# Kernel tuning notes

Measured on AMD Instinct MI355X. Metric: run time of the kernel, lower is better.

## Reference

```python
import jax, jax.numpy as jnp
import numpy as np

DIM, HEADS, MLP_RATIO = 384, 6, 4.0
HEAD_DIM = DIM // HEADS
HID = int(DIM * MLP_RATIO)
EPS = 1e-5


def _layer_norm(x, g, b):
    m = jnp.mean(x, axis=-1, keepdims=True)
    v = jnp.mean(jnp.square(x - m), axis=-1, keepdims=True)
    return (x - m) * jax.lax.rsqrt(v + EPS) * g + b


def setup_inputs() -> dict:
    key = jax.random.key(0)
    ks = jax.random.split(key, 16)
    B, N, C = 4, 2048, DIM
    s = 0.02
    return {
        "x": jax.random.normal(ks[0], (B, N, C), dtype=jnp.float32),
        "ln1_g": jnp.ones((C,), jnp.float32),
        "ln1_b": jnp.zeros((C,), jnp.float32),
        "qkv_w": jax.random.normal(ks[1], (C, 3 * C), jnp.float32) * s,  # [in, out]
        "qkv_b": jnp.zeros((3 * C,), jnp.float32),
        "proj_w": jax.random.normal(ks[2], (C, C), jnp.float32) * s,
        "proj_b": jnp.zeros((C,), jnp.float32),
        "ln2_g": jnp.ones((C,), jnp.float32),
        "ln2_b": jnp.zeros((C,), jnp.float32),
        "fc1_w": jax.random.normal(ks[3], (C, HID), jnp.float32) * s,
        "fc1_b": jnp.zeros((HID,), jnp.float32),
        "fc2_w": jax.random.normal(ks[4], (HID, C), jnp.float32) * s,
        "fc2_b": jnp.zeros((C,), jnp.float32),
    }


def reference(x, ln1_g, ln1_b, qkv_w, qkv_b, proj_w, proj_b,
              ln2_g, ln2_b, fc1_w, fc1_b, fc2_w, fc2_b):
    B, N, C = x.shape
    scale = HEAD_DIM ** (-0.5)

    # --- attention branch (pre-norm) ---
    h = _layer_norm(x, ln1_g, ln1_b)
    qkv = (h @ qkv_w + qkv_b).reshape(B, N, 3, HEADS, HEAD_DIM)
    qkv = jnp.transpose(qkv, (2, 0, 3, 1, 4))  # [3, B, H, N, D]
    q, k, v = qkv[0], qkv[1], qkv[2]
    attn = jnp.einsum("bhnd,bhmd->bhnm", q, k) * scale
    attn = jax.nn.softmax(attn, axis=-1)
    out = jnp.einsum("bhnm,bhmd->bhnd", attn, v)
    out = jnp.transpose(out, (0, 2, 1, 3)).reshape(B, N, C)
    x = x + (out @ proj_w + proj_b)

    # --- MLP branch (pre-norm) ---
    h = _layer_norm(x, ln2_g, ln2_b)
    h = jax.nn.gelu(h @ fc1_w + fc1_b, approximate=False)
    x = x + (h @ fc2_w + fc2_b)
    return x
```

## Files before the change

### kernel.cpp

```cpp
#include <hip/hip_runtime.h>

typedef unsigned short u16;
typedef unsigned int u32;
typedef __bf16 bf16x8_t __attribute__((ext_vector_type(8)));
typedef float f32x4 __attribute__((ext_vector_type(4)));
typedef float f32x16 __attribute__((ext_vector_type(16)));

__device__ __forceinline__ u16 f2b(float f) {
  union { float f; u32 u; } v; v.f = f;
  u32 r = v.u + 0x7fffu + ((v.u >> 16) & 1u);
  return (u16)(r >> 16);
}

__device__ __forceinline__ u32 pkbf(float a, float b) {
  union { __bf16 h[2]; u32 u; } v;
  v.h[0] = (__bf16)a; v.h[1] = (__bf16)b;
  return v.u;
}

__device__ __forceinline__ f32x4 mfma16(uint4 a, uint4 b, f32x4 c) {
  return __builtin_amdgcn_mfma_f32_16x16x32_bf16(
      __builtin_bit_cast(bf16x8_t, a), __builtin_bit_cast(bf16x8_t, b), c, 0, 0, 0);
}

__device__ __forceinline__ f32x16 mfma32(uint4 a, uint4 b, f32x16 c) {
  return __builtin_amdgcn_mfma_f32_32x32x16_bf16(
      __builtin_bit_cast(bf16x8_t, a), __builtin_bit_cast(bf16x8_t, b), c, 0, 0, 0);
}

__device__ __forceinline__ void plswap(u32& a, u32& b) {
  asm("v_permlane32_swap_b32 %0, %1" : "+v"(a), "+v"(b));
}

__device__ __forceinline__ void load_lds16(const void* g, void* l) {
  __builtin_amdgcn_global_load_lds(
      (const __attribute__((address_space(1))) unsigned int*)g,
      (__attribute__((address_space(3))) unsigned int*)l, 16, 0, 0);
}

template <int N>
__device__ __forceinline__ void waitvm() {
  if constexpr (N == 0) asm volatile("s_waitcnt vmcnt(0)" ::: "memory");
  else if constexpr (N == 2) asm volatile("s_waitcnt vmcnt(2)" ::: "memory");
  else if constexpr (N == 4) asm volatile("s_waitcnt vmcnt(4)" ::: "memory");
  else if constexpr (N == 6) asm volatile("s_waitcnt vmcnt(6)" ::: "memory");
  else asm volatile("s_waitcnt vmcnt(8)" ::: "memory");
}

__global__ __launch_bounds__(256) void convT4_k(
    const float* __restrict__ w0, u16* __restrict__ t0_,
    const float* __restrict__ w1, u16* __restrict__ t1_,
    const float* __restrict__ w2, u16* __restrict__ t2_,
    const float* __restrict__ w3, u16* __restrict__ t3_) {
  __shared__ u16 L[64][68];
  int tile = blockIdx.x, tid = threadIdx.x;
  const float* w; u16* wt; int K, N, rel;
  if (tile < 108)      { w = w0; wt = t0_; K = 384;  N = 1152; rel = tile; }
  else if (tile < 144) { w = w1; wt = t1_; K = 384;  N = 384;  rel = tile - 108; }
  else if (tile < 288) { w = w2; wt = t2_; K = 384;  N = 1536; rel = tile - 144; }
  else                 { w = w3; wt = t3_; K = 1536; N = 384;  rel = tile - 288; }
  int ntx = N >> 6;
  int tk = (rel / ntx) << 6, tn = (rel - (rel / ntx) * ntx) << 6;

  int r = tid >> 2, c0 = (tid & 3) << 4;
  const float* src = w + (size_t)(tk + r) * N + tn + c0;
#pragma unroll
  for (int j = 0; j < 16; j += 4) {
    float4 a = *(const float4*)(src + j);
    L[r][c0 + j + 0] = f2b(a.x);
    L[r][c0 + j + 1] = f2b(a.y);
    L[r][c0 + j + 2] = f2b(a.z);
    L[r][c0 + j + 3] = f2b(a.w);
  }
  __syncthreads();
  int n = tid >> 2, k0 = (tid & 3) << 4;
  u16 tmp[16];
#pragma unroll
  for (int j = 0; j < 16; j++) tmp[j] = L[k0 + j][n];
  u16* dst = wt + (size_t)(tn + n) * K + tk + k0;
  *(uint4*)dst = *(const uint4*)(tmp);
  *(uint4*)(dst + 8) = *(const uint4*)(tmp + 8);
}

__global__ __launch_bounds__(256) void ln_k(const float* __restrict__ x,
                                            const float* __restrict__ g,
                                            const float* __restrict__ bta,
                                            u16* __restrict__ out) {
  int lane = threadIdx.x & 63, wid = threadIdx.x >> 6;
  int row = blockIdx.x * 4 + wid;
  const float* xr = x + (size_t)row * 384;
  float v[6];
  float s = 0.f;
#pragma unroll
  for (int i = 0; i < 6; i++) { v[i] = xr[i * 64 + lane]; s += v[i]; }
#pragma unroll
  for (int off = 32; off >= 1; off >>= 1) s += __shfl_xor(s, off);
  float mean = s * (1.0f / 384.0f);
  float vs = 0.f;
#pragma unroll
  for (int i = 0; i < 6; i++) { float d = v[i] - mean; vs += d * d; }
#pragma unroll
  for (int off = 32; off >= 1; off >>= 1) vs += __shfl_xor(vs, off);
  float rstd = rsqrtf(vs * (1.0f / 384.0f) + 1e-5f);
  u16* orow = out + (size_t)row * 384;
#pragma unroll
  for (int i = 0; i < 6; i++) {
    int c = i * 64 + lane;
    orow[c] = f2b((v[i] - mean) * rstd * g[c] + bta[c]);
  }
}

template <int EPI, int MR, int NR>
__global__ __launch_bounds__(256, 3) void gemm_k(
    const u16* __restrict__ A, const u16* __restrict__ Bt,
    const float* __restrict__ bias, const float* __restrict__ res,
    void* __restrict__ outp, int M, int Nn, int K,
    u16* __restrict__ qp, u16* __restrict__ kp, u16* __restrict__ vtp) {
  constexpr int BMt = MR * 32;
  constexpr int BNt = NR * 32;
  constexpr int AW = MR / 2;
  constexpr int BW = NR / 2;
  __shared__ __align__(16) u16 As[3][BMt * 32];
  __shared__ __align__(16) u16 Bs[3][BNt * 32];
  int tid = threadIdx.x;
  int lane = tid & 63, wid = tid >> 6;
  int li = lane & 15, lg = lane >> 4;
  int wr = wid >> 1, wc = wid & 1;
  int row0 = blockIdx.y * BMt, col0 = blockIdx.x * BNt;

  int lr4 = lane >> 2;
  int sc4 = (((lane & 3) ^ (lr4 & 3) ^ ((lane >> 4) & 1))) * 8;

  f32x4 z = {0.f, 0.f, 0.f, 0.f};
  f32x4 acc[MR][NR];
#pragma unroll
  for (int m = 0; m < MR; m++)
#pragma unroll
    for (int n = 0; n < NR; n++) acc[m][n] = z;

  auto STAGE = [&](int buf, int k0) {
#pragma unroll
    for (int j = 0; j < AW; j++) {
      int ia = wid * AW + j;
      load_lds16(A + (size_t)(row0 + ia * 16 + lr4) * K + k0 + sc4,
                 (char*)As[buf] + ia * 1024);
    }
#pragma unroll
    for (int j = 0; j < BW; j++) {
      int ib = wid * BW + j;
      load_lds16(Bt + (size_t)(col0 + ib * 16 + lr4) * K + k0 + sc4,
                 (char*)Bs[buf] + ib * 1024);
    }
  };

  int nsteps = K >> 5;
  STAGE(0, 0);
  STAGE(1, 32);

  int cur = 0;
  for (int t = 0; t < nsteps; t++) {
    if (t + 1 < nsteps) waitvm<AW + BW>();
    else waitvm<0>();
    __builtin_amdgcn_s_barrier();
    asm volatile("" ::: "memory");
    if (t + 2 < nsteps) {
      int nx = cur + 2; if (nx >= 3) nx -= 3;
      STAGE(nx, (t + 2) * 32);
    }
    const char* Asb = (const char*)As[cur];
    const char* Bsb = (const char*)Bs[cur];
    uint4 af[MR], bf[NR];
#pragma unroll
    for (int m = 0; m < MR; m++) {
      int r = wr * (MR * 16) + m * 16 + li;
      af[m] = *(const uint4*)(
          Asb + r * 64 +
          ((lg * 16) ^ ((r & 3) << 4) ^ (((r >> 2) & 1) << 4)));
    }
#pragma unroll
    for (int n = 0; n < NR; n++) {
      int c = wc * (NR * 16) + n * 16 + li;
      bf[n] = *(const uint4*)(
          Bsb + c * 64 +
          ((lg * 16) ^ ((c & 3) << 4) ^ (((c >> 2) & 1) << 4)));
    }
#pragma unroll
    for (int m = 0; m < MR; m++)
#pragma unroll
      for (int n = 0; n < NR; n++)
        acc[m][n] = mfma16(af[m], bf[n], acc[m][n]);
    asm volatile("" ::: "memory");
    cur = (cur == 2) ? 0 : cur + 1;
  }

#pragma unroll
  for (int m = 0; m < MR; m++) {
#pragma unroll
    for (int n = 0; n < NR; n++) {
#pragma unroll
      for (int j = 0; j < 4; j++) {
        int r = row0 + wr * (MR * 16) + m * 16 + lg * 4 + j;
        int c = col0 + wc * (NR * 16) + n * 16 + li;
        float v = acc[m][n][j] + bias[c];
        if (EPI == 0) {
          ((float*)outp)[(size_t)r * Nn + c] = v + res[(size_t)r * Nn + c];
        } else if (EPI == 1) {
          float e = __expf(-1.5957691f * v * (1.f + 0.044715f * v * v));
          ((u16*)outp)[(size_t)r * Nn + c] = f2b(v / (1.f + e));
        } else {
          int t = c / 384;
          int c2 = c - t * 384;
          int hh = c2 >> 6, d = c2 & 63;
          int bb = r >> 11, nn = r & 2047;
          size_t bh = (size_t)bb * 6 + hh;
          int tile = nn >> 5;
          if (t == 2) {
            int kvl = nn & 31;
            int kvHalf = (kvl >> 4) & 1, h2 = (kvl >> 3) & 1, jj = kvl & 7;
            int dTile = d >> 5, l31 = d & 31;
            vtp[(((bh * 64 + tile) * 2 + dTile) * 2 + kvHalf) * 512 +
                (l31 + h2 * 32) * 8 + jj] = f2b(v);
          } else {
            int chunk = d >> 4, h2 = (d >> 3) & 1, e = d & 7;
            int l31 = nn & 31;
            size_t off = ((bh * 64 + tile) * 4 + chunk) * 512 +
                         (l31 + h2 * 32) * 8 + e;
            if (t == 0) qp[off] = f2b(v * 0.18033688f);
            else        kp[off] = f2b(v);
          }
        }
      }
    }
  }
}

__global__ __launch_bounds__(256, 3) void attn_k(const u16* __restrict__ q,
                                                 const u16* __restrict__ k,
                                                 const u16* __restrict__ vt,
                                                 u16* __restrict__ out) {
  __shared__ __align__(16) float Ol[3][2][16][64];
  __shared__ float Ls[3][64];

  int tid = threadIdx.x;
  int lane = tid & 63, wid = tid >> 6;
  int l31 = lane & 31, hi = lane >> 5;
  int bid = blockIdx.x;
  int nid = (bid & 7) * 192 + (bid >> 3);
  int bh = nid >> 6, qT = nid & 63;
  int b = bh / 6, hh = bh - b * 6;
  int qb = qT * 32;

  const u16* qp_ = q + ((size_t)bh * 64 + qT) * 2048 + lane * 8;
  const u16* kp_ = k + ((size_t)bh * 64 + wid * 16) * 2048 + lane * 8;
  const u16* vp_ = vt + ((size_t)bh * 64 + wid * 16) * 2048 + lane * 8;

  uint4 qf[4], kf[4], vf[4];
#pragma unroll
  for (int c = 0; c < 4; c++) qf[c] = *(const uint4*)(qp_ + c * 512);
#pragma unroll
  for (int c = 0; c < 4; c++) kf[c] = *(const uint4*)(kp_ + c * 512);
#pragma unroll
  for (int c = 0; c < 4; c++) vf[c] = *(const uint4*)(vp_ + c * 512);
  kp_ += 2048;
  vp_ += 2048;

  f32x16 o0, o1;
#pragma unroll
  for (int r = 0; r < 16; r++) { o0[r] = 0.f; o1[r] = 0.f; }
  float lsum = 0.f;

#pragma unroll
  for (int t = 0; t < 16; t++) {
    uint4 kn[4], vn[4];
    if (t < 15) {
#pragma unroll
      for (int c = 0; c < 4; c++) kn[c] = *(const uint4*)(kp_ + c * 512);
#pragma unroll
      for (int c = 0; c < 4; c++) vn[c] = *(const uint4*)(vp_ + c * 512);
    }

    f32x16 s;
#pragma unroll
    for (int r = 0; r < 16; r++) s[r] = 0.f;
#pragma unroll
    for (int c = 0; c < 4; c++) s = mfma32(kf[c], qf[c], s);

    float p[16];
#pragma unroll
    for (int r = 0; r < 16; r++) p[r] = __builtin_amdgcn_exp2f(s[r]);
    lsum += ((p[0] + p[1]) + (p[2] + p[3])) + ((p[4] + p[5]) + (p[6] + p[7])) +
            ((p[8] + p[9]) + (p[10] + p[11])) +
            ((p[12] + p[13]) + (p[14] + p[15]));

    u32 u[8];
#pragma unroll
    for (int i = 0; i < 8; i++) u[i] = pkbf(p[2 * i], p[2 * i + 1]);
    plswap(u[0], u[2]); plswap(u[1], u[3]);
    plswap(u[4], u[6]); plswap(u[5], u[7]);
    uint4 pa0 = {u[0], u[1], u[2], u[3]};
    uint4 pa1 = {u[4], u[5], u[6], u[7]};

    o0 = mfma32(pa0, vf[0], o0);
    o0 = mfma32(pa1, vf[1], o0);
    o1 = mfma32(pa0, vf[2], o1);
    o1 = mfma32(pa1, vf[3], o1);

    if (t < 15) {
#pragma unroll
      for (int c = 0; c < 4; c++) { kf[c] = kn[c]; vf[c] = vn[c]; }
    }
    kp_ += 2048;
    vp_ += 2048;
  }

  lsum += __shfl_xor(lsum, 32);

  if (wid) {
#pragma unroll
    for (int r = 0; r < 16; r++) {
      Ol[wid - 1][0][r][lane] = o0[r];
      Ol[wid - 1][1][r][lane] = o1[r];
    }
    Ls[wid - 1][lane] = lsum;
  }
  __syncthreads();
  if (wid == 0) {
#pragma unroll
    for (int w = 0; w < 3; w++) lsum += Ls[w][lane];
#pragma unroll
    for (int r = 0; r < 16; r++)
#pragma unroll
      for (int w = 0; w < 3; w++) {
        o0[r] += Ol[w][0][r][lane];
        o1[r] += Ol[w][1][r][lane];
      }
    float rl = 1.0f / lsum;
#pragma unroll
    for (int r = 0; r < 16; r++) {
      int qo = (r & 3) + 8 * (r >> 2) + hi * 4;
      float rlq = __shfl(rl, qo, 64);
      int row = b * 2048 + qb + qo;
      out[(size_t)row * 384 + hh * 64 + l31] = f2b(o0[r] * rlq);
      out[(size_t)row * 384 + hh * 64 + 32 + l31] = f2b(o1[r] * rlq);
    }
  }
}

extern "C" void kernel_launch(void* const* d_in, const int* in_sizes, int n_in,
                              void* d_out, int out_size, void* d_ws,
                              size_t ws_size, hipStream_t stream) {
  const float* x      = (const float*)d_in[0];
  const float* ln1_g  = (const float*)d_in[1];
  const float* ln1_b  = (const float*)d_in[2];
  const float* qkv_w  = (const float*)d_in[3];
  const float* qkv_b  = (const float*)d_in[4];
  const float* proj_w = (const float*)d_in[5];
  const float* proj_b = (const float*)d_in[6];
  const float* ln2_g  = (const float*)d_in[7];
  const float* ln2_b  = (const float*)d_in[8];
  const float* fc1_w  = (const float*)d_in[9];
  const float* fc1_b  = (const float*)d_in[10];
  const float* fc2_w  = (const float*)d_in[11];
  const float* fc2_b  = (const float*)d_in[12];
  float* out = (float*)d_out;

  char* p = (char*)d_ws;
  u16* qkvwt  = (u16*)p;  p += (size_t)1152 * 384 * 2;
  u16* projwt = (u16*)p;  p += (size_t)384 * 384 * 2;
  u16* fc1wt  = (u16*)p;  p += (size_t)1536 * 384 * 2;
  u16* fc2wt  = (u16*)p;  p += (size_t)384 * 1536 * 2;
  float* x1   = (float*)p; p += (size_t)8192 * 384 * 4;
  u16* reg1   = (u16*)p;  p += (size_t)8192 * 384 * 2;
  u16* reg2   = (u16*)p;  p += (size_t)8192 * 1536 * 2;
  u16* qd  = reg2;
  u16* kd  = reg2 + (size_t)24 * 2048 * 64;
  u16* vtd = kd + (size_t)24 * 2048 * 64;
  u16* h3  = reg2;

  convT4_k<<<432, 256, 0, stream>>>(qkv_w, qkvwt, proj_w, projwt,
                                    fc1_w, fc1wt, fc2_w, fc2wt);

  ln_k<<<2048, 256, 0, stream>>>(x, ln1_g, ln1_b, reg1);
  gemm_k<2, 4, 4><<<dim3(9, 64), 256, 0, stream>>>(
      reg1, qkvwt, qkv_b, nullptr, nullptr, 8192, 1152, 384, qd, kd, vtd);
  attn_k<<<dim3(1536), 256, 0, stream>>>(qd, kd, vtd, reg1);
  gemm_k<0, 2, 2><<<dim3(6, 128), 256, 0, stream>>>(
      reg1, projwt, proj_b, x, x1, 8192, 384, 384, nullptr, nullptr, nullptr);
  ln_k<<<2048, 256, 0, stream>>>(x1, ln2_g, ln2_b, reg1);
  gemm_k<1, 4, 4><<<dim3(12, 64), 256, 0, stream>>>(
      reg1, fc1wt, fc1_b, nullptr, h3, 8192, 1536, 384, nullptr, nullptr, nullptr);
  gemm_k<0, 2, 2><<<dim3(6, 128), 256, 0, stream>>>(
      h3, fc2wt, fc2_b, x1, out, 8192, 384, 1536, nullptr, nullptr, nullptr);
}
```

Before: 147.8 us.

## Store activations in MFMA fragment-major layout and load A directly to registers

LayerNorm, attention output and the fc1 GELU epilogue now write bf16 activations in a 16x8 fragment-major tiled layout. The GEMM loads A fragments straight from global memory into registers, double-buffered, and stages only B through LDS with 64-wide K steps. The N tile is fixed at 64, K is a compile-time template parameter, and occupancy hints rise to 4 for the GEMM and 6 for attention. This is meant to cut LDS traffic and barrier work for A. The cost is more, smaller blocks for the QKV and fc1 GEMMs and uncoalesced-looking epilogue stores.

```diff
diff --git a/kernel.cpp b/kernel.cpp
--- a/kernel.cpp
+++ b/kernel.cpp
@@ -18,6 +18,10 @@
   return v.u;
 }
 
+__device__ __forceinline__ size_t fmoff(int r, int c, int Kd) {
+  return ((size_t)(r >> 4) * (Kd >> 3) + (c >> 3)) * 128 + (r & 15) * 8 + (c & 7);
+}
+
 __device__ __forceinline__ f32x4 mfma16(uint4 a, uint4 b, f32x4 c) {
   return __builtin_amdgcn_mfma_f32_16x16x32_bf16(
       __builtin_bit_cast(bf16x8_t, a), __builtin_bit_cast(bf16x8_t, b), c, 0, 0, 0);
@@ -36,15 +40,6 @@
   __builtin_amdgcn_global_load_lds(
       (const __attribute__((address_space(1))) unsigned int*)g,
       (__attribute__((address_space(3))) unsigned int*)l, 16, 0, 0);
-}
-
-template <int N>
-__device__ __forceinline__ void waitvm() {
-  if constexpr (N == 0) asm volatile("s_waitcnt vmcnt(0)" ::: "memory");
-  else if constexpr (N == 2) asm volatile("s_waitcnt vmcnt(2)" ::: "memory");
-  else if constexpr (N == 4) asm volatile("s_waitcnt vmcnt(4)" ::: "memory");
-  else if constexpr (N == 6) asm volatile("s_waitcnt vmcnt(6)" ::: "memory");
-  else asm volatile("s_waitcnt vmcnt(8)" ::: "memory");
 }
 
 __global__ __launch_bounds__(256) void convT4_k(
@@ -102,119 +97,115 @@
 #pragma unroll
   for (int off = 32; off >= 1; off >>= 1) vs += __shfl_xor(vs, off);
   float rstd = rsqrtf(vs * (1.0f / 384.0f) + 1e-5f);
-  u16* orow = out + (size_t)row * 384;
 #pragma unroll
   for (int i = 0; i < 6; i++) {
     int c = i * 64 + lane;
-    orow[c] = f2b((v[i] - mean) * rstd * g[c] + bta[c]);
-  }
-}
-
-template <int EPI, int MR, int NR>
-__global__ __launch_bounds__(256, 3) void gemm_k(
+    out[fmoff(row, c, 384)] = f2b((v[i] - mean) * rstd * g[c] + bta[c]);
+  }
+}
+
+template <int EPI, int MR, int KD>
+__global__ __launch_bounds__(256, 4) void gemm_k(
     const u16* __restrict__ A, const u16* __restrict__ Bt,
     const float* __restrict__ bias, const float* __restrict__ res,
-    void* __restrict__ outp, int M, int Nn, int K,
+    void* __restrict__ outp, int Nn,
     u16* __restrict__ qp, u16* __restrict__ kp, u16* __restrict__ vtp) {
   constexpr int BMt = MR * 32;
-  constexpr int BNt = NR * 32;
-  constexpr int AW = MR / 2;
-  constexpr int BW = NR / 2;
-  __shared__ __align__(16) u16 As[3][BMt * 32];
-  __shared__ __align__(16) u16 Bs[3][BNt * 32];
+  constexpr int NS = KD / 64;
+  constexpr int KD8 = KD / 8;
+  __shared__ __align__(16) u16 Bs[2][64 * 64];
   int tid = threadIdx.x;
   int lane = tid & 63, wid = tid >> 6;
   int li = lane & 15, lg = lane >> 4;
   int wr = wid >> 1, wc = wid & 1;
-  int row0 = blockIdx.y * BMt, col0 = blockIdx.x * BNt;
-
-  int lr4 = lane >> 2;
-  int sc4 = (((lane & 3) ^ (lr4 & 3) ^ ((lane >> 4) & 1))) * 8;
+  int row0 = blockIdx.y * BMt, col0 = blockIdx.x * 64;
+
+  int lr = lane >> 3;
+  int sc8 = ((lane & 7) ^ lr) * 8;
+
+  const u16* Ab = A + ((size_t)(row0 / 16 + wr * MR) * KD8 + lg) * 128 + li * 8;
 
   f32x4 z = {0.f, 0.f, 0.f, 0.f};
-  f32x4 acc[MR][NR];
+  f32x4 acc[MR][2];
 #pragma unroll
   for (int m = 0; m < MR; m++)
 #pragma unroll
-    for (int n = 0; n < NR; n++) acc[m][n] = z;
-
-  auto STAGE = [&](int buf, int k0) {
-#pragma unroll
-    for (int j = 0; j < AW; j++) {
-      int ia = wid * AW + j;
-      load_lds16(A + (size_t)(row0 + ia * 16 + lr4) * K + k0 + sc4,
-                 (char*)As[buf] + ia * 1024);
-    }
-#pragma unroll
-    for (int j = 0; j < BW; j++) {
-      int ib = wid * BW + j;
-      load_lds16(Bt + (size_t)(col0 + ib * 16 + lr4) * K + k0 + sc4,
+    for (int n = 0; n < 2; n++) acc[m][n] = z;
+
+  uint4 af[2][MR][2];
+
+  auto stageB = [&](int buf, int k0) {
+#pragma unroll
+    for (int j = 0; j < 2; j++) {
+      int ib = wid * 2 + j;
+      load_lds16(Bt + (size_t)(col0 + ib * 8 + lr) * KD + k0 + sc8,
                  (char*)Bs[buf] + ib * 1024);
     }
   };
-
-  int nsteps = K >> 5;
-  STAGE(0, 0);
-  STAGE(1, 32);
-
-  int cur = 0;
-  for (int t = 0; t < nsteps; t++) {
-    if (t + 1 < nsteps) waitvm<AW + BW>();
-    else waitvm<0>();
-    __builtin_amdgcn_s_barrier();
-    asm volatile("" ::: "memory");
-    if (t + 2 < nsteps) {
-      int nx = cur + 2; if (nx >= 3) nx -= 3;
-      STAGE(nx, (t + 2) * 32);
-    }
-    const char* Asb = (const char*)As[cur];
-    const char* Bsb = (const char*)Bs[cur];
-    uint4 af[MR], bf[NR];
-#pragma unroll
-    for (int m = 0; m < MR; m++) {
-      int r = wr * (MR * 16) + m * 16 + li;
-      af[m] = *(const uint4*)(
-          Asb + r * 64 +
-          ((lg * 16) ^ ((r & 3) << 4) ^ (((r >> 2) & 1) << 4)));
-    }
-#pragma unroll
-    for (int n = 0; n < NR; n++) {
-      int c = wc * (NR * 16) + n * 16 + li;
-      bf[n] = *(const uint4*)(
-          Bsb + c * 64 +
-          ((lg * 16) ^ ((c & 3) << 4) ^ (((c >> 2) & 1) << 4)));
-    }
+  auto loadA = [&](uint4 (*dst)[2], int cc0) {
 #pragma unroll
     for (int m = 0; m < MR; m++)
 #pragma unroll
-      for (int n = 0; n < NR; n++)
-        acc[m][n] = mfma16(af[m], bf[n], acc[m][n]);
-    asm volatile("" ::: "memory");
-    cur = (cur == 2) ? 0 : cur + 1;
+      for (int kk = 0; kk < 2; kk++)
+        dst[m][kk] =
+            *(const uint4*)(Ab + ((size_t)m * KD8 + cc0 + kk * 4) * 128);
+  };
+
+  stageB(0, 0);
+  loadA(af[0], 0);
+  asm volatile("s_waitcnt vmcnt(0)" ::: "memory");
+  __builtin_amdgcn_s_barrier();
+
+#pragma unroll
+  for (int t = 0; t < NS; t++) {
+    if (t + 1 < NS) {
+      stageB((t + 1) & 1, (t + 1) * 64);
+      loadA(af[(t + 1) & 1], (t + 1) * 8);
+    }
+    const char* Bsb = (const char*)Bs[t & 1];
+#pragma unroll
+    for (int kk = 0; kk < 2; kk++) {
+      uint4 bf[2];
+#pragma unroll
+      for (int n = 0; n < 2; n++) {
+        int c = wc * 32 + n * 16 + li;
+        bf[n] = *(const uint4*)(Bsb + c * 128 +
+                                ((kk * 64 + lg * 16) ^ ((c & 7) << 4)));
+      }
+#pragma unroll
+      for (int m = 0; m < MR; m++)
+#pragma unroll
+        for (int n = 0; n < 2; n++)
+          acc[m][n] = mfma16(af[t & 1][m][kk], bf[n], acc[m][n]);
+    }
+    if (t + 1 < NS) {
+      asm volatile("s_waitcnt vmcnt(0)" ::: "memory");
+      __builtin_amdgcn_s_barrier();
+    }
   }
 
 #pragma unroll
   for (int m = 0; m < MR; m++) {
 #pragma unroll
-    for (int n = 0; n < NR; n++) {
+    for (int n = 0; n < 2; n++) {
 #pragma unroll
       for (int j = 0; j < 4; j++) {
         int r = row0 + wr * (MR * 16) + m * 16 + lg * 4 + j;
-        int c = col0 + wc * (NR * 16) + n * 16 + li;
+        int c = col0 + wc * 32 + n * 16 + li;
         float v = acc[m][n][j] + bias[c];
         if (EPI == 0) {
           ((float*)outp)[(size_t)r * Nn + c] = v + res[(size_t)r * Nn + c];
         } else if (EPI == 1) {
           float e = __expf(-1.5957691f * v * (1.f + 0.044715f * v * v));
-          ((u16*)outp)[(size_t)r * Nn + c] = f2b(v / (1.f + e));
+          ((u16*)outp)[fmoff(r, c, Nn)] = f2b(v / (1.f + e));
         } else {
-          int t = c / 384;
-          int c2 = c - t * 384;
+          int tt = c / 384;
+          int c2 = c - tt * 384;
           int hh = c2 >> 6, d = c2 & 63;
           int bb = r >> 11, nn = r & 2047;
           size_t bh = (size_t)bb * 6 + hh;
           int tile = nn >> 5;
-          if (t == 2) {
+          if (tt == 2) {
             int kvl = nn & 31;
             int kvHalf = (kvl >> 4) & 1, h2 = (kvl >> 3) & 1, jj = kvl & 7;
             int dTile = d >> 5, l31 = d & 31;
@@ -225,8 +216,8 @@
             int l31 = nn & 31;
             size_t off = ((bh * 64 + tile) * 4 + chunk) * 512 +
                          (l31 + h2 * 32) * 8 + e;
-            if (t == 0) qp[off] = f2b(v * 0.18033688f);
-            else        kp[off] = f2b(v);
+            if (tt == 0) qp[off] = f2b(v * 0.18033688f);
+            else         kp[off] = f2b(v);
           }
         }
       }
@@ -234,7 +225,7 @@
   }
 }
 
-__global__ __launch_bounds__(256, 3) void attn_k(const u16* __restrict__ q,
+__global__ __launch_bounds__(256, 6) void attn_k(const u16* __restrict__ q,
                                                  const u16* __restrict__ k,
                                                  const u16* __restrict__ vt,
                                                  u16* __restrict__ out) {
@@ -340,8 +331,8 @@
       int qo = (r & 3) + 8 * (r >> 2) + hi * 4;
       float rlq = __shfl(rl, qo, 64);
       int row = b * 2048 + qb + qo;
-      out[(size_t)row * 384 + hh * 64 + l31] = f2b(o0[r] * rlq);
-      out[(size_t)row * 384 + hh * 64 + 32 + l31] = f2b(o1[r] * rlq);
+      out[fmoff(row, hh * 64 + l31, 384)] = f2b(o0[r] * rlq);
+      out[fmoff(row, hh * 64 + 32 + l31, 384)] = f2b(o1[r] * rlq);
     }
   }
 }
@@ -381,14 +372,14 @@
                                     fc1_w, fc1wt, fc2_w, fc2wt);
 
   ln_k<<<2048, 256, 0, stream>>>(x, ln1_g, ln1_b, reg1);
-  gemm_k<2, 4, 4><<<dim3(9, 64), 256, 0, stream>>>(
-      reg1, qkvwt, qkv_b, nullptr, nullptr, 8192, 1152, 384, qd, kd, vtd);
+  gemm_k<2, 4, 384><<<dim3(18, 64), 256, 0, stream>>>(
+      reg1, qkvwt, qkv_b, nullptr, nullptr, 1152, qd, kd, vtd);
   attn_k<<<dim3(1536), 256, 0, stream>>>(qd, kd, vtd, reg1);
-  gemm_k<0, 2, 2><<<dim3(6, 128), 256, 0, stream>>>(
-      reg1, projwt, proj_b, x, x1, 8192, 384, 384, nullptr, nullptr, nullptr);
+  gemm_k<0, 2, 384><<<dim3(6, 128), 256, 0, stream>>>(
+      reg1, projwt, proj_b, x, x1, 384, nullptr, nullptr, nullptr);
   ln_k<<<2048, 256, 0, stream>>>(x1, ln2_g, ln2_b, reg1);
-  gemm_k<1, 4, 4><<<dim3(12, 64), 256, 0, stream>>>(
-      reg1, fc1wt, fc1_b, nullptr, h3, 8192, 1536, 384, nullptr, nullptr, nullptr);
-  gemm_k<0, 2, 2><<<dim3(6, 128), 256, 0, stream>>>(
-      h3, fc2wt, fc2_b, x1, out, 8192, 384, 1536, nullptr, nullptr, nullptr);
-}
+  gemm_k<1, 4, 384><<<dim3(24, 64), 256, 0, stream>>>(
+      reg1, fc1wt, fc1_b, nullptr, h3, 1536, nullptr, nullptr, nullptr);
+  gemm_k<0, 2, 1536><<<dim3(6, 128), 256, 0, stream>>>(
+      h3, fc2wt, fc2_b, x1, out, 384, nullptr, nullptr, nullptr);
+}
```

Result: slower. 363.8 us (+146.1%).
